# Kernel optimization log

Measured on AMD Instinct MI355X. Metric: run time of the kernel, lower is better.

The kernel has to match this reference:

```python
import jax, jax.numpy as jnp
import numpy as np

L = 4        # initial_layers (layers actually run in forward)
DIM = 128    # model dim
NB = 8       # num_blocks per layer
K = 2        # max_active blocks per layer
B = 131072   # batch
FIN = 32     # input features (nn.Linear(32, dim))
PRIORITY = 0.5  # fresh block: success_rate*0.6 + excitement*0.4 = 0.5


def setup_inputs() -> dict:
    key = jax.random.key(0)
    ks = jax.random.split(key, 10)
    s = 0.02
    return {
        "x": jax.random.normal(ks[0], (B, FIN), dtype=jnp.float32),
        "proj_w": jax.random.normal(ks[1], (FIN, DIM)) * s,
        "proj_b": jnp.zeros((DIM,)),
        "pos": jax.random.normal(ks[2], (1, 16, DIM)) * 0.02,
        "sel_w": jax.random.normal(ks[3], (L, DIM, NB)) * s,   # per-layer selector
        "sel_b": jnp.zeros((L, NB)),
        "ln_s": jnp.ones((L, NB, DIM)),                         # per-block LayerNorm
        "ln_b": jnp.zeros((L, NB, DIM)),
        "w1": jax.random.normal(ks[4], (L, NB, DIM, 2 * DIM)) * s,
        "b1": jnp.zeros((L, NB, 2 * DIM)),
        "w2": jax.random.normal(ks[5], (L, NB, 2 * DIM, DIM)) * s,
        "b2": jnp.zeros((L, NB, DIM)),
        "gate": jax.random.normal(ks[6], (L, NB, DIM)) * 0.01,  # torsion_gate
        "cls_w": jax.random.normal(ks[7], (DIM, 2)) * s,
        "cls_b": jnp.zeros((2,)),
        "torsion_field": jnp.zeros((1, DIM)),                   # registered buffer (zeros)
    }


def _block(h, ln_s, ln_b, w1, b1, w2, b2, gate, tf):
    # h: [B, 1, DIM]. LayerNorm(eps=1e-5) -> Linear -> GELU -> Linear -> torsion gate -> 0.5 residual
    mu = h.mean(axis=-1, keepdims=True)
    var = ((h - mu) ** 2).mean(axis=-1, keepdims=True)
    hn = (h - mu) / jnp.sqrt(var + 1e-5) * ln_s + ln_b
    z = jax.nn.gelu(hn @ w1 + b1, approximate=False) @ w2 + b2
    te = jax.nn.sigmoid(gate) * tf           # [1, DIM]
    z = z * (1.0 + te[:, None, :])           # broadcast over seq dim (unsqueeze(1))
    return h + 0.5 * z


def reference(x, proj_w, proj_b, pos, sel_w, sel_b, ln_s, ln_b,
              w1, b1, w2, b2, gate, cls_w, cls_b, torsion_field):
    # input projection + positional slice; seq_len == 1
    h = (x @ proj_w + proj_b)[:, None, :] + pos[:, :1, :]   # [B, 1, DIM]
    for l in range(L):
        scores = jax.nn.sigmoid(h.mean(axis=1) @ sel_w[l] + sel_b[l])  # [B, NB]
        # adjusted[0, i] = scores[0, i]*0.6 + priority*0.4 ; top-k taken on row 0
        adj = scores[0] * 0.6 + PRIORITY * 0.4
        _, top = jax.lax.top_k(adj, K)
        for k in range(K):
            i = top[k]
            h = _block(h, ln_s[l][i], ln_b[l][i], w1[l][i], b1[l][i],
                       w2[l][i], b2[l][i], gate[l][i], torsion_field)
    logits = h.mean(axis=1) @ cls_w + cls_b   # [B, 2]
    return logits, h
```

## Files before the change

kernel.cpp:

```cpp
#include <hip/hip_runtime.h>


typedef __attribute__((ext_vector_type(8))) short s16x8;
typedef __attribute__((ext_vector_type(4))) float f32x4;
typedef unsigned short ushort_t;

#define BATCH 131072
#define TBROWS 32
#define HSTR 132
#define FGSTR 544
#define FQSTR 136

#define WS_IDX 0
#define WS_PRM 64
#define WS_PB  12352
#define WS_PW  12864
#define WS_W1  21056
#define WS_W2  545344
#define WS_DMP 1069632

__device__ inline ushort_t f2bf(float f) {
  unsigned u = __float_as_uint(f);
  u += 0x7fffu + ((u >> 16) & 1u);
  return (ushort_t)(u >> 16);
}
__device__ inline ushort_t f2bf1(float f) {
  return (ushort_t)((__float_as_uint(f) + 0x8000u) >> 16);
}
__device__ inline unsigned f2bf2(float lo, float hi) {
  unsigned a = __float_as_uint(lo) + 0x8000u;
  unsigned b = __float_as_uint(hi) + 0x8000u;
  return __builtin_amdgcn_perm(b, a, 0x07060302u);
}

__device__ inline float dpp_xor1(float v) {
  return __int_as_float(__builtin_amdgcn_update_dpp(
      0, __float_as_int(v), 0xB1 , 0xF, 0xF, true));
}
__device__ inline float dpp_xor2(float v) {
  return __int_as_float(__builtin_amdgcn_update_dpp(
      0, __float_as_int(v), 0x4E , 0xF, 0xF, true));
}

__device__ inline float geluf(float v) {
  float e = __builtin_amdgcn_exp2f(-2.4554670f * v);
  return v * __builtin_amdgcn_rcpf(1.0f + e);
}

__global__ __launch_bounds__(256) void uv6_warm(
    const float* __restrict__ w1, const float* __restrict__ w2,
    float* __restrict__ dump) {
  int gid = blockIdx.x * 256 + threadIdx.x;
  const float4* a = (const float4*)w1;
  const float4* b = (const float4*)w2;
  float s = 0.0f;
#pragma unroll
  for (int i = 0; i < 2; ++i) {
    float4 v = a[gid + i * 131072];
    float4 u = b[gid + i * 131072];
    s += v.x + v.y + v.z + v.w + u.x + u.y + u.z + u.w;
  }
  if (s > 1e30f) dump[0] = s;
}

__global__ __launch_bounds__(1024) void uv6_select(
    const float* __restrict__ x, const float* __restrict__ proj_w,
    const float* __restrict__ proj_b, const float* __restrict__ pos,
    const float* __restrict__ sel_w, const float* __restrict__ sel_b,
    const float* __restrict__ ln_s, const float* __restrict__ ln_b,
    const float* __restrict__ w1, const float* __restrict__ b1,
    const float* __restrict__ w2, const float* __restrict__ b2,
    const float* __restrict__ gate, const float* __restrict__ tf,
    int* __restrict__ wsI) {
  __shared__ float h0[128], hn[128], z1[256];
  __shared__ float red[1024];
  __shared__ float wred[128];
  __shared__ float adjs[8];
  __shared__ int top[2];
  __shared__ float stat[2];
  const int t = threadIdx.x;
  const int lane = t & 63, wv = t >> 6;
  const int n1 = t & 255, dp1 = t >> 8;
  const int n2 = t & 127, dp2 = t >> 7;

  if (t < 128) {
    float a = proj_b[t] + pos[t];
#pragma unroll
    for (int f = 0; f < 32; ++f) a += x[f] * proj_w[f * 128 + t];
    h0[t] = a;
  }
  __syncthreads();

  for (int l = 0; l < 4; ++l) {
    {
      float pp = h0[t >> 3] * sel_w[(l * 128 + (t >> 3)) * 8 + (t & 7)];
      pp += __shfl_xor(pp, 8);
      pp += __shfl_xor(pp, 16);
      pp += __shfl_xor(pp, 32);
      if (lane < 8) wred[wv * 8 + lane] = pp;
    }
    __syncthreads();
    if (t < 8) {
      float sc = sel_b[l * 8 + t];
#pragma unroll
      for (int v = 0; v < 16; ++v) sc += wred[v * 8 + t];
      sc = 1.0f / (1.0f + __expf(-sc));
      adjs[t] = sc * 0.6f + 0.2f;
    }
    __syncthreads();
    if (t == 0) {
      int i0 = 0; float v0 = adjs[0];
      for (int j = 1; j < 8; ++j) if (adjs[j] > v0) { v0 = adjs[j]; i0 = j; }
      int i1 = -1; float v1 = -1e30f;
      for (int j = 0; j < 8; ++j) if (j != i0 && adjs[j] > v1) { v1 = adjs[j]; i1 = j; }
      top[0] = i0; top[1] = i1;
      wsI[2 * l] = i0; wsI[2 * l + 1] = i1;
    }
    __syncthreads();
    for (int kk = 0; kk < 2; ++kk) {
      const int base = l * 8 + top[kk];
      float w1v[32], w2v[32];
      const float* w1p = w1 + (base * 128 + dp1 * 32) * 256 + n1;
      const float* w2p = w2 + (base * 256 + dp2 * 32) * 128 + n2;
#pragma unroll
      for (int j = 0; j < 32; ++j) w1v[j] = w1p[j * 256];
#pragma unroll
      for (int j = 0; j < 32; ++j) w2v[j] = w2p[j * 128];
      if (t < 64) {
        float a = h0[t], b = h0[t + 64];
        float s2 = a + b, q2 = a * a + b * b;
        s2 += __shfl_xor(s2, 1);  q2 += __shfl_xor(q2, 1);
        s2 += __shfl_xor(s2, 2);  q2 += __shfl_xor(q2, 2);
        s2 += __shfl_xor(s2, 4);  q2 += __shfl_xor(q2, 4);
        s2 += __shfl_xor(s2, 8);  q2 += __shfl_xor(q2, 8);
        s2 += __shfl_xor(s2, 16); q2 += __shfl_xor(q2, 16);
        s2 += __shfl_xor(s2, 32); q2 += __shfl_xor(q2, 32);
        if (t == 0) {
          float mu = s2 * (1.0f / 128.0f);
          stat[0] = mu;
          stat[1] = rsqrtf(q2 * (1.0f / 128.0f) - mu * mu + 1e-5f);
        }
      }
      __syncthreads();
      if (t < 128)
        hn[t] = (h0[t] - stat[0]) * stat[1] * ln_s[base * 128 + t] + ln_b[base * 128 + t];
      __syncthreads();
      {
        float a = 0.0f;
#pragma unroll
        for (int j = 0; j < 32; ++j) a += hn[dp1 * 32 + j] * w1v[j];
        red[dp1 * 256 + n1] = a;
      }
      __syncthreads();
      if (t < 256) {
        float z = red[t] + red[256 + t] + red[512 + t] + red[768 + t] + b1[base * 256 + t];
        z1[t] = z * 0.5f * (1.0f + erff(z * 0.70710678118f));
      }
      __syncthreads();
      {
        float a = 0.0f;
#pragma unroll
        for (int j = 0; j < 32; ++j) a += z1[dp2 * 32 + j] * w2v[j];
        red[dp2 * 128 + n2] = a;
      }
      __syncthreads();
      if (t < 128) {
        float z2 = b2[base * 128 + t];
#pragma unroll
        for (int v = 0; v < 8; ++v) z2 += red[v * 128 + t];
        float te = tf[t] * (1.0f / (1.0f + __expf(-gate[base * 128 + t])));
        h0[t] += 0.5f * z2 * (1.0f + te);
      }
      __syncthreads();
    }
  }
}

__global__ __launch_bounds__(256) void uv6_pack(
    const float* __restrict__ w1, const float* __restrict__ w2,
    const float* __restrict__ ln_s, const float* __restrict__ ln_b,
    const float* __restrict__ b1, const float* __restrict__ b2,
    const float* __restrict__ gate, const float* __restrict__ tf,
    const float* __restrict__ proj_w, const float* __restrict__ proj_b,
    const float* __restrict__ pos, const int* __restrict__ wsI,
    ushort_t* __restrict__ w1P, ushort_t* __restrict__ w2P,
    float* __restrict__ wsP, ushort_t* __restrict__ pwP,
    float* __restrict__ pb) {
  const int bx = blockIdx.x;
  if (bx < 2048) {
    int gid = bx * 256 + threadIdx.x;
    int s = gid >> 16, e = gid & 65535;
    int base = (s >> 1) * 8 + wsI[s];
    if (e < 32768) {
      int j = e & 7, ln = (e >> 3) & 63, ks = (e >> 9) & 3, nt = e >> 11;
      int k = ks * 32 + (ln >> 4) * 8 + j;
      int n = nt * 16 + (ln & 15);
      w1P[s * 32768 + e] = f2bf(w1[(base * 128 + k) * 256 + n] * ln_s[base * 128 + k]);
    } else {
      int e2 = e - 32768;
      int j = e2 & 7, ln = (e2 >> 3) & 63, ks = (e2 >> 9) & 7, nt = e2 >> 12;
      int k = ks * 32 + (ln >> 4) * 8 + j;
      int n = nt * 16 + (ln & 15);
      float te = tf[n] * (1.0f / (1.0f + __expf(-gate[base * 128 + n])));
      w2P[s * 32768 + e2] = f2bf(w2[(base * 256 + k) * 128 + n] * (0.5f * (1.0f + te)));
    }
    return;
  }
  if (bx < 2056) {
    int s = bx - 2048, n = threadIdx.x;
    int base = (s >> 1) * 8 + wsI[s];
    float a = b1[base * 256 + n];
#pragma unroll 16
    for (int k = 0; k < 128; ++k)
      a += ln_b[base * 128 + k] * w1[(base * 128 + k) * 256 + n];
    wsP[s * 384 + n] = a;
    if (n < 128) {
      float te = tf[n] * (1.0f / (1.0f + __expf(-gate[base * 128 + n])));
      wsP[s * 384 + 256 + n] = 0.5f * (1.0f + te) * b2[base * 128 + n];
    }
    return;
  }
  int gid = (bx - 2056) * 256 + threadIdx.x;
  if (gid < 4096) {
    int j = gid & 7, ln = (gid >> 3) & 63, nt = gid >> 9;
    int k = (ln >> 4) * 8 + j, n = nt * 16 + (ln & 15);
    pwP[gid] = f2bf(proj_w[k * 128 + n]);
  } else if (gid < 4224) {
    int d = gid - 4096;
    pb[d] = proj_b[d] + pos[d];
  }
}

__global__ __launch_bounds__(256, 4) void uv6_main(
    const float* __restrict__ x, const float* __restrict__ cls_w,
    const float* __restrict__ cls_b, const float* __restrict__ wsP,
    const float* __restrict__ pb, const ushort_t* __restrict__ pwP,
    const ushort_t* __restrict__ w1P, const ushort_t* __restrict__ w2P,
    float* __restrict__ out) {
  __shared__ float hbuf[TBROWS * HSTR];
  __shared__ ushort_t frag[16 * FGSTR];

  const int tid = threadIdx.x;
  const int w = tid >> 6, lane = tid & 63, q = lane >> 4, m0 = lane & 15;
  const int r = tid >> 3, p = tid & 7;
  const int rt_r = r >> 4, m_r = r & 15;
  const long rowbase = (long)blockIdx.x * TBROWS;

  {
    float4 xv = *(const float4*)(x + (rowbase + r) * 32 + p * 4);
    unsigned u01 = f2bf2(xv.x, xv.y), u23 = f2bf2(xv.z, xv.w);
    ushort_t* dst = &frag[(rt_r * 8) * FGSTR + (p >> 1) * FQSTR + m_r * 8 + (p & 1) * 4];
    *(unsigned*)dst = u01;
    *(unsigned*)(dst + 2) = u23;
  }
  __syncthreads();

  {
    s16x8 bp0 = *(const s16x8*)(pwP + ((2 * w + 0) * 64 + lane) * 8);
    s16x8 bp1 = *(const s16x8*)(pwP + ((2 * w + 1) * 64 + lane) * 8);
    float bv0 = pb[(2 * w + 0) * 16 + m0];
    float bv1 = pb[(2 * w + 1) * 16 + m0];
    f32x4 acc[2][2];
#pragma unroll
    for (int rt = 0; rt < 2; ++rt) {
      acc[rt][0] = (f32x4){bv0, bv0, bv0, bv0};
      acc[rt][1] = (f32x4){bv1, bv1, bv1, bv1};
    }
#pragma unroll
    for (int rt = 0; rt < 2; ++rt) {
      s16x8 af = *(const s16x8*)&frag[(rt * 8) * FGSTR + q * FQSTR + m0 * 8];
      acc[rt][0] = __builtin_amdgcn_mfma_f32_16x16x32_bf16(af, bp0, acc[rt][0], 0, 0, 0);
      acc[rt][1] = __builtin_amdgcn_mfma_f32_16x16x32_bf16(af, bp1, acc[rt][1], 0, 0, 0);
    }
#pragma unroll
    for (int rt = 0; rt < 2; ++rt)
#pragma unroll
      for (int ni = 0; ni < 2; ++ni) {
        int col = (2 * w + ni) * 16 + m0;
#pragma unroll
        for (int reg = 0; reg < 4; ++reg)
          hbuf[(rt * 16 + 4 * q + reg) * HSTR + col] = acc[rt][ni][reg];
      }
  }
  __syncthreads();

  float* outH = out + (size_t)BATCH * 2;

  for (int s = 0; s < 8; ++s) {
    const float* c1 = wsP + s * 384;
    const float* c2 = c1 + 256;
    const ushort_t* w1s = w1P + s * 32768;
    const ushort_t* w2s = w2P + s * 32768;

    s16x8 bfr1[4][4];
#pragma unroll
    for (int ni = 0; ni < 4; ++ni)
#pragma unroll
      for (int ks = 0; ks < 4; ++ks)
        bfr1[ni][ks] = *(const s16x8*)(w1s + (((4 * w + ni) * 4 + ks) * 64 + lane) * 8);

    {
      const float* hr = hbuf + r * HSTR + p * 16;
      float hv[16];
#pragma unroll
      for (int i = 0; i < 4; ++i)
        *(float4*)(hv + i * 4) = *(const float4*)(hr + i * 4);
      float sum = 0.0f, ssq = 0.0f;
#pragma unroll
      for (int i = 0; i < 16; ++i) { sum += hv[i]; ssq += hv[i] * hv[i]; }
      sum += dpp_xor1(sum); ssq += dpp_xor1(ssq);
      sum += dpp_xor2(sum); ssq += dpp_xor2(ssq);
      sum += __shfl_xor(sum, 4); ssq += __shfl_xor(ssq, 4);
      float mu = sum * (1.0f / 128.0f);
      float rstd = rsqrtf(ssq * (1.0f / 128.0f) - mu * mu + 1e-5f);
      float nmu = -mu * rstd;
#pragma unroll
      for (int g = 0; g < 2; ++g) {
        union { unsigned u[4]; s16x8 v; } tv;
#pragma unroll
        for (int jj = 0; jj < 4; ++jj) {
          float a = fmaf(hv[g * 8 + jj * 2], rstd, nmu);
          float b = fmaf(hv[g * 8 + jj * 2 + 1], rstd, nmu);
          tv.u[jj] = f2bf2(a, b);
        }
        int kb = p >> 1, kq = (p & 1) * 2 + g;
        *(s16x8*)&frag[(rt_r * 8 + kb) * FGSTR + kq * FQSTR + m_r * 8] = tv.v;
      }
    }
    __syncthreads();

    f32x4 a1[2][4];
#pragma unroll
    for (int ni = 0; ni < 4; ++ni) {
      float bv = c1[(4 * w + ni) * 16 + m0];
#pragma unroll
      for (int rt = 0; rt < 2; ++rt) a1[rt][ni] = (f32x4){bv, bv, bv, bv};
    }
#pragma unroll
    for (int ks = 0; ks < 4; ++ks) {
      s16x8 af[2];
#pragma unroll
      for (int rt = 0; rt < 2; ++rt)
        af[rt] = *(const s16x8*)&frag[(rt * 8 + ks) * FGSTR + q * FQSTR + m0 * 8];
#pragma unroll
      for (int rt = 0; rt < 2; ++rt)
#pragma unroll
        for (int ni = 0; ni < 4; ++ni)
          a1[rt][ni] = __builtin_amdgcn_mfma_f32_16x16x32_bf16(af[rt], bfr1[ni][ks], a1[rt][ni], 0, 0, 0);
    }
    __syncthreads();

    s16x8 bfr2[2][8];
#pragma unroll
    for (int ni = 0; ni < 2; ++ni)
#pragma unroll
      for (int ks = 0; ks < 8; ++ks)
        bfr2[ni][ks] = *(const s16x8*)(w2s + (((2 * w + ni) * 8 + ks) * 64 + lane) * 8);
    float cv0 = c2[(2 * w + 0) * 16 + m0];
    float cv1 = c2[(2 * w + 1) * 16 + m0];

    {
      int j = m0 & 7;
#pragma unroll
      for (int ni = 0; ni < 4; ++ni) {
        int kb = 2 * w + (ni >> 1);
        int kq = (2 * ni + (m0 >> 3)) & 3;
#pragma unroll
        for (int rt = 0; rt < 2; ++rt)
#pragma unroll
          for (int reg = 0; reg < 4; ++reg)
            frag[(rt * 8 + kb) * FGSTR + kq * FQSTR + (4 * q + reg) * 8 + j] =
                f2bf1(geluf(a1[rt][ni][reg]));
      }
    }
    __syncthreads();

    f32x4 a2[2][2];
#pragma unroll
    for (int rt = 0; rt < 2; ++rt) {
      a2[rt][0] = (f32x4){cv0, cv0, cv0, cv0};
      a2[rt][1] = (f32x4){cv1, cv1, cv1, cv1};
    }
#pragma unroll
    for (int kb = 0; kb < 8; ++kb) {
      s16x8 af[2];
#pragma unroll
      for (int rt = 0; rt < 2; ++rt)
        af[rt] = *(const s16x8*)&frag[(rt * 8 + kb) * FGSTR + q * FQSTR + m0 * 8];
#pragma unroll
      for (int rt = 0; rt < 2; ++rt) {
        a2[rt][0] = __builtin_amdgcn_mfma_f32_16x16x32_bf16(af[rt], bfr2[0][kb], a2[rt][0], 0, 0, 0);
        a2[rt][1] = __builtin_amdgcn_mfma_f32_16x16x32_bf16(af[rt], bfr2[1][kb], a2[rt][1], 0, 0, 0);
      }
    }

#pragma unroll
    for (int rt = 0; rt < 2; ++rt)
#pragma unroll
      for (int ni = 0; ni < 2; ++ni) {
        int col = (2 * w + ni) * 16 + m0;
#pragma unroll
        for (int reg = 0; reg < 4; ++reg)
          hbuf[(rt * 16 + 4 * q + reg) * HSTR + col] += a2[rt][ni][reg];
      }
    __syncthreads();
  }

#pragma unroll
  for (int it = 0; it < 4; ++it) {
    int p4 = it * 256 + tid;
    int row = p4 >> 5, c = (p4 & 31) * 4;
    float4 o = *(const float4*)(hbuf + row * HSTR + c);
    *(float4*)(outH + rowbase * 128 + p4 * 4) = o;
  }

  {
    const float* hr = hbuf + r * HSTR + p * 16;
    float l0 = 0.0f, l1 = 0.0f;
#pragma unroll
    for (int i = 0; i < 16; i += 4) {
      float4 v = *(const float4*)(hr + i);
      int c = (p * 16 + i) * 2;
      l0 += v.x * cls_w[c] + v.y * cls_w[c + 2] + v.z * cls_w[c + 4] + v.w * cls_w[c + 6];
      l1 += v.x * cls_w[c + 1] + v.y * cls_w[c + 3] + v.z * cls_w[c + 5] + v.w * cls_w[c + 7];
    }
    l0 += dpp_xor1(l0); l1 += dpp_xor1(l1);
    l0 += dpp_xor2(l0); l1 += dpp_xor2(l1);
    l0 += __shfl_xor(l0, 4); l1 += __shfl_xor(l1, 4);
    if (p == 0) {
      float2 lg = {l0 + cls_b[0], l1 + cls_b[1]};
      *(float2*)(out + (rowbase + r) * 2) = lg;
    }
  }
}

extern "C" void kernel_launch(void* const* d_in, const int* in_sizes, int n_in,
                              void* d_out, int out_size, void* d_ws, size_t ws_size,
                              hipStream_t stream) {
  (void)in_sizes; (void)n_in; (void)out_size; (void)ws_size;
  const float* x      = (const float*)d_in[0];
  const float* proj_w = (const float*)d_in[1];
  const float* proj_b = (const float*)d_in[2];
  const float* pos    = (const float*)d_in[3];
  const float* sel_w  = (const float*)d_in[4];
  const float* sel_b  = (const float*)d_in[5];
  const float* ln_s   = (const float*)d_in[6];
  const float* ln_b   = (const float*)d_in[7];
  const float* w1     = (const float*)d_in[8];
  const float* b1     = (const float*)d_in[9];
  const float* w2     = (const float*)d_in[10];
  const float* b2     = (const float*)d_in[11];
  const float* gate   = (const float*)d_in[12];
  const float* cls_w  = (const float*)d_in[13];
  const float* cls_b  = (const float*)d_in[14];
  const float* tf     = (const float*)d_in[15];

  char* ws = (char*)d_ws;
  int* wsI        = (int*)(ws + WS_IDX);
  float* wsP      = (float*)(ws + WS_PRM);
  float* pb       = (float*)(ws + WS_PB);
  ushort_t* pwP   = (ushort_t*)(ws + WS_PW);
  ushort_t* w1P   = (ushort_t*)(ws + WS_W1);
  ushort_t* w2P   = (ushort_t*)(ws + WS_W2);
  float* dump     = (float*)(ws + WS_DMP);
  float* outF     = (float*)d_out;

  uv6_warm<<<512, 256, 0, stream>>>(w1, w2, dump);
  uv6_select<<<1, 1024, 0, stream>>>(x, proj_w, proj_b, pos, sel_w, sel_b, ln_s,
                                     ln_b, w1, b1, w2, b2, gate, tf, wsI);
  uv6_pack<<<2073, 256, 0, stream>>>(w1, w2, ln_s, ln_b, b1, b2, gate, tf,
                                     proj_w, proj_b, pos, wsI, w1P, w2P, wsP,
                                     pwP, pb);
  uv6_main<<<BATCH / TBROWS, 256, 0, stream>>>(x, cls_w, cls_b, wsP, pb, pwP,
                                               w1P, w2P, outF);
}
```

Measured before the change: 368.3 us.

## Tile weight packing through LDS and transpose first GEMM to vectorize GELU stores

The pack kernel now uses 16 blocks that read weights with coalesced float4 loads, reorder them into the MFMA fragment layout in shared memory, and write out 16-byte chunks, instead of 2048 blocks doing scattered per-element gathers. In the main kernel the first MFMA swaps its A and B operands so each lane holds four consecutive hidden columns. That lets the GELU output be packed and stored as 8-byte vectors rather than single bf16 scalar stores, and the bias loads become vector loads. The trade-off is far fewer blocks in packing, so less parallelism there.

```diff
diff --git a/kernel.cpp b/kernel.cpp
--- a/kernel.cpp
+++ b/kernel.cpp
@@ -3,6 +3,7 @@
 
 typedef __attribute__((ext_vector_type(8))) short s16x8;
 typedef __attribute__((ext_vector_type(4))) float f32x4;
+typedef __attribute__((ext_vector_type(2))) unsigned u32x2;
 typedef unsigned short ushort_t;
 
 #define BATCH 131072
@@ -187,27 +188,71 @@
     float* __restrict__ wsP, ushort_t* __restrict__ pwP,
     float* __restrict__ pb) {
   const int bx = blockIdx.x;
-  if (bx < 2048) {
-    int gid = bx * 256 + threadIdx.x;
-    int s = gid >> 16, e = gid & 65535;
+  const int t = threadIdx.x;
+  if (bx < 16) {
+    __shared__ ushort_t tile[32768];
+    int s = bx >> 1;
     int base = (s >> 1) * 8 + wsI[s];
-    if (e < 32768) {
-      int j = e & 7, ln = (e >> 3) & 63, ks = (e >> 9) & 3, nt = e >> 11;
-      int k = ks * 32 + (ln >> 4) * 8 + j;
-      int n = nt * 16 + (ln & 15);
-      w1P[s * 32768 + e] = f2bf(w1[(base * 128 + k) * 256 + n] * ln_s[base * 128 + k]);
+    if ((bx & 1) == 0) {
+      const float* W = w1 + base * 32768;
+      const float* LS = ln_s + base * 128;
+      int kk = t >> 6, n4 = (t & 63) * 4;
+#pragma unroll
+      for (int it = 0; it < 16; ++it) {
+        int k = it * 8 + kk * 2;
+        float4 v0 = *(const float4*)(W + k * 256 + n4);
+        float4 v1 = *(const float4*)(W + (k + 1) * 256 + n4);
+        float s0 = LS[k], s1 = LS[k + 1];
+        int pk = (k >> 5) * 512 + ((k >> 3) & 3) * 128 + (k & 7);
+        const float* e0 = (const float*)&v0;
+        const float* e1 = (const float*)&v1;
+#pragma unroll
+        for (int i = 0; i < 4; ++i) {
+          int n = n4 + i;
+          int pos_ = (n >> 4) * 2048 + pk + (n & 15) * 8;
+          *(unsigned*)&tile[pos_] =
+              (unsigned)f2bf(e0[i] * s0) | ((unsigned)f2bf(e1[i] * s1) << 16);
+        }
+      }
+      __syncthreads();
+      ushort_t* dst = w1P + s * 32768;
+#pragma unroll
+      for (int it = 0; it < 16; ++it)
+        *(uint4*)(dst + (it * 256 + t) * 8) = *(const uint4*)(tile + (it * 256 + t) * 8);
     } else {
-      int e2 = e - 32768;
-      int j = e2 & 7, ln = (e2 >> 3) & 63, ks = (e2 >> 9) & 7, nt = e2 >> 12;
-      int k = ks * 32 + (ln >> 4) * 8 + j;
-      int n = nt * 16 + (ln & 15);
-      float te = tf[n] * (1.0f / (1.0f + __expf(-gate[base * 128 + n])));
-      w2P[s * 32768 + e2] = f2bf(w2[(base * 256 + k) * 128 + n] * (0.5f * (1.0f + te)));
+      const float* W = w2 + base * 32768;
+      int kk = t >> 5, n4 = (t & 31) * 4;
+      float te4[4];
+#pragma unroll
+      for (int i = 0; i < 4; ++i)
+        te4[i] = 0.5f * (1.0f + tf[n4 + i] *
+                 (1.0f / (1.0f + __expf(-gate[base * 128 + n4 + i]))));
+#pragma unroll
+      for (int it = 0; it < 16; ++it) {
+        int k = it * 16 + kk * 2;
+        float4 v0 = *(const float4*)(W + k * 128 + n4);
+        float4 v1 = *(const float4*)(W + (k + 1) * 128 + n4);
+        int pk = (k >> 5) * 512 + ((k >> 3) & 3) * 128 + (k & 7);
+        const float* e0 = (const float*)&v0;
+        const float* e1 = (const float*)&v1;
+#pragma unroll
+        for (int i = 0; i < 4; ++i) {
+          int n = n4 + i;
+          int pos_ = (n >> 4) * 4096 + pk + (n & 15) * 8;
+          *(unsigned*)&tile[pos_] =
+              (unsigned)f2bf(e0[i] * te4[i]) | ((unsigned)f2bf(e1[i] * te4[i]) << 16);
+        }
+      }
+      __syncthreads();
+      ushort_t* dst = w2P + s * 32768;
+#pragma unroll
+      for (int it = 0; it < 16; ++it)
+        *(uint4*)(dst + (it * 256 + t) * 8) = *(const uint4*)(tile + (it * 256 + t) * 8);
     }
     return;
   }
-  if (bx < 2056) {
-    int s = bx - 2048, n = threadIdx.x;
+  if (bx < 24) {
+    int s = bx - 16, n = t;
     int base = (s >> 1) * 8 + wsI[s];
     float a = b1[base * 256 + n];
 #pragma unroll 16
@@ -220,7 +265,7 @@
     }
     return;
   }
-  int gid = (bx - 2056) * 256 + threadIdx.x;
+  int gid = (bx - 24) * 256 + t;
   if (gid < 4096) {
     int j = gid & 7, ln = (gid >> 3) & 63, nt = gid >> 9;
     int k = (ln >> 4) * 8 + j, n = nt * 16 + (ln & 15);
@@ -245,6 +290,7 @@
   const int r = tid >> 3, p = tid & 7;
   const int rt_r = r >> 4, m_r = r & 15;
   const long rowbase = (long)blockIdx.x * TBROWS;
+  ushort_t* fb = &frag[q * FQSTR + m0 * 8];
 
   {
     float4 xv = *(const float4*)(x + (rowbase + r) * 32 + p * 4);
@@ -268,7 +314,7 @@
     }
 #pragma unroll
     for (int rt = 0; rt < 2; ++rt) {
-      s16x8 af = *(const s16x8*)&frag[(rt * 8) * FGSTR + q * FQSTR + m0 * 8];
+      s16x8 af = *(const s16x8*)&fb[(rt * 8) * FGSTR];
       acc[rt][0] = __builtin_amdgcn_mfma_f32_16x16x32_bf16(af, bp0, acc[rt][0], 0, 0, 0);
       acc[rt][1] = __builtin_amdgcn_mfma_f32_16x16x32_bf16(af, bp1, acc[rt][1], 0, 0, 0);
     }
@@ -332,21 +378,21 @@
     f32x4 a1[2][4];
 #pragma unroll
     for (int ni = 0; ni < 4; ++ni) {
-      float bv = c1[(4 * w + ni) * 16 + m0];
-#pragma unroll
-      for (int rt = 0; rt < 2; ++rt) a1[rt][ni] = (f32x4){bv, bv, bv, bv};
+      f32x4 bv = *(const f32x4*)&c1[(4 * w + ni) * 16 + 4 * q];
+#pragma unroll
+      for (int rt = 0; rt < 2; ++rt) a1[rt][ni] = bv;
     }
 #pragma unroll
     for (int ks = 0; ks < 4; ++ks) {
-      s16x8 af[2];
+      s16x8 hf[2];
 #pragma unroll
       for (int rt = 0; rt < 2; ++rt)
-        af[rt] = *(const s16x8*)&frag[(rt * 8 + ks) * FGSTR + q * FQSTR + m0 * 8];
+        hf[rt] = *(const s16x8*)&fb[(rt * 8 + ks) * FGSTR];
 #pragma unroll
       for (int rt = 0; rt < 2; ++rt)
 #pragma unroll
         for (int ni = 0; ni < 4; ++ni)
-          a1[rt][ni] = __builtin_amdgcn_mfma_f32_16x16x32_bf16(af[rt], bfr1[ni][ks], a1[rt][ni], 0, 0, 0);
+          a1[rt][ni] = __builtin_amdgcn_mfma_f32_16x16x32_bf16(bfr1[ni][ks], hf[rt], a1[rt][ni], 0, 0, 0);
     }
     __syncthreads();
 
@@ -360,17 +406,18 @@
     float cv1 = c2[(2 * w + 1) * 16 + m0];
 
     {
-      int j = m0 & 7;
+      int j0 = 4 * (q & 1), kqb = q >> 1;
 #pragma unroll
       for (int ni = 0; ni < 4; ++ni) {
         int kb = 2 * w + (ni >> 1);
-        int kq = (2 * ni + (m0 >> 3)) & 3;
-#pragma unroll
-        for (int rt = 0; rt < 2; ++rt)
-#pragma unroll
-          for (int reg = 0; reg < 4; ++reg)
-            frag[(rt * 8 + kb) * FGSTR + kq * FQSTR + (4 * q + reg) * 8 + j] =
-                f2bf1(geluf(a1[rt][ni][reg]));
+        int kq = (2 * ni + kqb) & 3;
+#pragma unroll
+        for (int rt = 0; rt < 2; ++rt) {
+          unsigned lo = f2bf2(geluf(a1[rt][ni][0]), geluf(a1[rt][ni][1]));
+          unsigned hi = f2bf2(geluf(a1[rt][ni][2]), geluf(a1[rt][ni][3]));
+          *(u32x2*)&frag[(rt * 8 + kb) * FGSTR + kq * FQSTR + m0 * 8 + j0] =
+              (u32x2){lo, hi};
+        }
       }
     }
     __syncthreads();
@@ -386,7 +433,7 @@
       s16x8 af[2];
 #pragma unroll
       for (int rt = 0; rt < 2; ++rt)
-        af[rt] = *(const s16x8*)&frag[(rt * 8 + kb) * FGSTR + q * FQSTR + m0 * 8];
+        af[rt] = *(const s16x8*)&fb[(rt * 8 + kb) * FGSTR];
 #pragma unroll
       for (int rt = 0; rt < 2; ++rt) {
         a2[rt][0] = __builtin_amdgcn_mfma_f32_16x16x32_bf16(af[rt], bfr2[0][kb], a2[rt][0], 0, 0, 0);
@@ -468,9 +515,9 @@
   uv6_warm<<<512, 256, 0, stream>>>(w1, w2, dump);
   uv6_select<<<1, 1024, 0, stream>>>(x, proj_w, proj_b, pos, sel_w, sel_b, ln_s,
                                      ln_b, w1, b1, w2, b2, gate, tf, wsI);
-  uv6_pack<<<2073, 256, 0, stream>>>(w1, w2, ln_s, ln_b, b1, b2, gate, tf,
-                                     proj_w, proj_b, pos, wsI, w1P, w2P, wsP,
-                                     pwP, pb);
+  uv6_pack<<<41, 256, 0, stream>>>(w1, w2, ln_s, ln_b, b1, b2, gate, tf,
+                                   proj_w, proj_b, pos, wsI, w1P, w2P, wsP,
+                                   pwP, pb);
   uv6_main<<<BATCH / TBROWS, 256, 0, stream>>>(x, cls_w, cls_b, wsP, pb, pwP,
                                                w1P, w2P, outF);
 }
```

After: 362.8 us. Within noise of the previous version (-1.5%).
